# Performance work log

Hardware: AMD Instinct MI355X
Metric: run time of the kernel (lower is better)

The kernel has to match this reference:

```python
import jax, jax.numpy as jnp
import numpy as np

D_MODEL = 1024
N_HEADS = 16
D_HIDDEN = 4096
EPS = 1e-6
MASK_VAL = 1e10


def layernorm(x, gamma, beta):
    # Matches torch module: unbiased std (N-1), divide by (std + eps)
    mean = jnp.mean(x, axis=-1, keepdims=True)
    d = x.shape[-1]
    std = jnp.sqrt(jnp.sum((x - mean) ** 2, axis=-1, keepdims=True) / (d - 1))
    return gamma * (x - mean) / (std + EPS) + beta


def multihead(q_in, k_in, v_in, wq, wk, wv, wo, causal):
    # nn.Linear(bias=False): y = x @ W.T
    q = q_in @ wq.T
    k = k_in @ wk.T
    v = v_in @ wv.T
    B, Sq, D = q.shape
    Sk = k.shape[1]
    H, dh = N_HEADS, D // N_HEADS
    q = q.reshape(B, Sq, H, dh)
    k = k.reshape(B, Sk, H, dh)
    v = v.reshape(B, Sk, H, dh)
    scores = jnp.einsum('bqhd,bkhd->bhqk', q, k)  # [B,H,Sq,Sk]
    if causal:
        tri = jnp.triu(jnp.full((Sk, Sk), MASK_VAL, dtype=scores.dtype), k=1)
        scores = scores - tri  # mask applied BEFORE scaling, as in source
    scale = jnp.sqrt(jnp.asarray(D_MODEL, dtype=scores.dtype))  # d_key = d_model
    att = jax.nn.softmax(scores / scale, axis=-1)
    out = jnp.einsum('bhqk,bkhd->bqhd', att, v).reshape(B, Sq, D)
    return out @ wo.T


def setup_inputs() -> dict:
    key = jax.random.key(0)
    ks = jax.random.split(key, 24)
    B, S, D, DH = 2, 2048, D_MODEL, D_HIDDEN
    w = lambda k, shp: (jax.random.normal(k, shp, dtype=jnp.float32) * 0.02)
    inp = {
        'x': jax.random.normal(ks[0], (B, S, D), dtype=jnp.float32),
        'encoding': jax.random.normal(ks[1], (B, S, D), dtype=jnp.float32),
        'sa_wq': w(ks[2], (D, D)), 'sa_wk': w(ks[3], (D, D)),
        'sa_wv': w(ks[4], (D, D)), 'sa_wo': w(ks[5], (D, D)),
        'ca_wq': w(ks[6], (D, D)), 'ca_wk': w(ks[7], (D, D)),
        'ca_wv': w(ks[8], (D, D)), 'ca_wo': w(ks[9], (D, D)),
        'ff_w1': w(ks[10], (DH, D)), 'ff_b1': jnp.zeros((DH,), jnp.float32),
        'ff_w2': w(ks[11], (D, DH)), 'ff_b2': jnp.zeros((D,), jnp.float32),
        'ln1_g': jnp.ones((D,), jnp.float32), 'ln1_b': jnp.zeros((D,), jnp.float32),
        'ln2_g': jnp.ones((D,), jnp.float32), 'ln2_b': jnp.zeros((D,), jnp.float32),
        'ln3_g': jnp.ones((D,), jnp.float32), 'ln3_b': jnp.zeros((D,), jnp.float32),
    }
    return inp


def reference(x, encoding, sa_wq, sa_wk, sa_wv, sa_wo, ca_wq, ca_wk, ca_wv, ca_wo,
              ff_w1, ff_b1, ff_w2, ff_b2, ln1_g, ln1_b, ln2_g, ln2_b, ln3_g, ln3_b):
    # self-attention (causal) + post-norm residual
    h = layernorm(x + multihead(x, x, x, sa_wq, sa_wk, sa_wv, sa_wo, causal=True), ln1_g, ln1_b)
    # cross-attention + post-norm residual
    h = layernorm(h + multihead(h, encoding, encoding, ca_wq, ca_wk, ca_wv, ca_wo, causal=False), ln2_g, ln2_b)
    # feed-forward + post-norm residual
    ff = jax.nn.relu(h @ ff_w1.T + ff_b1) @ ff_w2.T + ff_b2
    return layernorm(h + ff, ln3_g, ln3_b)
```

## Files before the change

### kernel.cpp

```cpp
#include <hip/hip_runtime.h>
#include <hip/hip_bf16.h>
#include <math.h>

#define D_MODEL 1024
#define NHEADS  16
#define DHEAD   64
#define D_HID   4096

typedef __attribute__((ext_vector_type(8))) short short8;
typedef __attribute__((ext_vector_type(4))) short short4v;
typedef __attribute__((ext_vector_type(4))) float f32x4;
typedef __attribute__((ext_vector_type(16))) float f32x16;

#define QSCALE_F 0.04508422002778011f
#define MASK_T   4.5084220e8f

__device__ inline short f2bs(float x) {
    union { __hip_bfloat16 b; short s; } u;
    u.b = __float2bfloat16(x);
    return u.s;
}
__device__ inline float bs2f(ushort s) {
    union { unsigned u; float f; } v; v.u = ((unsigned)s) << 16; return v.f;
}
__device__ inline unsigned cvtpk(float lo, float hi) {
    unsigned r;
    asm("v_cvt_pk_bf16_f32 %0, %1, %2" : "=v"(r) : "v"(lo), "v"(hi));
    return r;
}
__device__ inline short8 pack8(float4 x, float4 y) {
    short8 v;
    v[0] = f2bs(x.x); v[1] = f2bs(x.y); v[2] = f2bs(x.z); v[3] = f2bs(x.w);
    v[4] = f2bs(y.x); v[5] = f2bs(y.y); v[6] = f2bs(y.z); v[7] = f2bs(y.w);
    return v;
}
typedef const unsigned __attribute__((address_space(1))) gu32;
typedef unsigned __attribute__((address_space(3))) lu32;
__device__ inline void gload16(const void* g, void* l) {
    __builtin_amdgcn_global_load_lds((gu32*)g, (lu32*)l, 16, 0, 0);
}
__device__ inline int swz(int r, int byteInRow) {
    return (r * 128 + byteInRow) ^ ((r & 7) << 4);
}

struct WP { const float* p[10]; };
__global__ __launch_bounds__(256) void cast_weights(WP wp, short* __restrict__ dst) {
    const int n8 = (16 << 20) / 8;
    for (int i = blockIdx.x * 256 + threadIdx.x; i < n8; i += gridDim.x * 256) {
        size_t e = (size_t)i * 8;
        int seg = (int)(e >> 20);
        const float* src;
        if (seg < 8)       src = wp.p[seg] + (e & ((1u << 20) - 1));
        else if (seg < 12) src = wp.p[8] + (e - ((size_t)8 << 20));
        else               src = wp.p[9] + (e - ((size_t)12 << 20));
        float4 a = *(const float4*)src;
        float4 b = *(const float4*)(src + 4);
        *(short8*)(dst + e) = pack8(a, b);
    }
}

__global__ __launch_bounds__(256) void cast_f2b(const float* __restrict__ in,
                                                short* __restrict__ out, int n8) {
    for (int i = blockIdx.x * 256 + threadIdx.x; i < n8; i += gridDim.x * 256) {
        float4 a = *(const float4*)(in + (size_t)i * 8);
        float4 b = *(const float4*)(in + (size_t)i * 8 + 4);
        *(short8*)(out + (size_t)i * 8) = pack8(a, b);
    }
}

template<int OM, bool BIAS, bool RELU, bool ACCUM>
__global__ __launch_bounds__(256) void gemm_mfma(
    const short* __restrict__ A, int lda,
    const short* __restrict__ Bm, int ldb,
    const float* __restrict__ bias,
    float* __restrict__ Cf, short* __restrict__ Cb, int ldc,
    int M, int N, int K, size_t routeElems, float qscale)
{
    __shared__ short Als[2][128 * 64];
    __shared__ short Bls[2][128 * 64];

    const int tid = threadIdx.x, w = tid >> 6, l = tid & 63;
    const int l15 = l & 15, lhi = l >> 4;
    const int wr = w >> 1, wc = w & 1;

    const int kh = (OM == 3) ? blockIdx.z : 0;
    if (OM == 3) {
        A  += (size_t)kh * K;
        Bm += (size_t)kh * K;
    }

    const unsigned nwg  = gridDim.x * gridDim.y;
    const unsigned wgid = blockIdx.y * gridDim.x + blockIdx.x;
    const unsigned cpx  = nwg >> 3;
    const unsigned sid  = (wgid & 7) * cpx + (wgid >> 3);
    const int bm = (int)(sid / gridDim.x) * 128;
    const int bn = (int)(sid % gridDim.x) * 128;

    const int srow = w * 8 + (l >> 3);
    const int schk = ((l & 7) ^ (l >> 3)) * 8;

    f32x4 acc[4][4] = {};

    #pragma unroll
    for (int i = 0; i < 4; ++i) {
        const short* ga = A  + (size_t)(bm + i * 32 + srow) * lda + schk;
        const short* gb = Bm + (size_t)(bn + i * 32 + srow) * ldb + schk;
        gload16(ga, &Als[0][i * 2048 + w * 512]);
        gload16(gb, &Bls[0][i * 2048 + w * 512]);
    }
    __syncthreads();

    const int nIter = K >> 6;
    int cur = 0;
    for (int it = 0; it < nIter; ++it) {
        if (it + 1 < nIter) {
            const int k1 = (it + 1) << 6;
            #pragma unroll
            for (int i = 0; i < 4; ++i) {
                const short* ga = A  + (size_t)(bm + i * 32 + srow) * lda + k1 + schk;
                const short* gb = Bm + (size_t)(bn + i * 32 + srow) * ldb + k1 + schk;
                gload16(ga, &Als[cur ^ 1][i * 2048 + w * 512]);
                gload16(gb, &Bls[cur ^ 1][i * 2048 + w * 512]);
            }
        }

        short8 af[4][2], bf[4][2];
        #pragma unroll
        for (int m = 0; m < 4; ++m) {
            const int row = wr * 64 + m * 16 + l15;
            #pragma unroll
            for (int kk = 0; kk < 2; ++kk)
                af[m][kk] = *(const short8*)&Als[cur][row * 64 + (((kk * 4 + lhi) ^ (l15 & 7)) * 8)];
        }
        #pragma unroll
        for (int n = 0; n < 4; ++n) {
            const int row = wc * 64 + n * 16 + l15;
            #pragma unroll
            for (int kk = 0; kk < 2; ++kk)
                bf[n][kk] = *(const short8*)&Bls[cur][row * 64 + (((kk * 4 + lhi) ^ (l15 & 7)) * 8)];
        }
        __builtin_amdgcn_s_setprio(1);
        #pragma unroll
        for (int kk = 0; kk < 2; ++kk)
            #pragma unroll
            for (int m = 0; m < 4; ++m)
                #pragma unroll
                for (int n = 0; n < 4; ++n)
                    acc[m][n] = __builtin_amdgcn_mfma_f32_16x16x32_bf16(af[m][kk], bf[n][kk], acc[m][n], 0, 0, 0);
        __builtin_amdgcn_s_setprio(0);

        __syncthreads();
        cur ^= 1;
    }

    #pragma unroll
    for (int n = 0; n < 4; ++n) {
        const int col = bn + wc * 64 + n * 16 + l15;
        float bv = 0.f;
        if (BIAS && (OM != 3 || kh == 0)) bv = bias[col];
        const float sc = (OM == 2) ? (col < 1024 ? qscale : 1.f) : qscale;
        #pragma unroll
        for (int m = 0; m < 4; ++m) {
            const int row0 = bm + wr * 64 + m * 16 + lhi * 4;
            #pragma unroll
            for (int i = 0; i < 4; ++i) {
                float v = acc[m][n][i] + bv;
                if (ACCUM) v += Cf[(size_t)(row0 + i) * ldc + col];
                if (RELU)  v = fmaxf(v, 0.f);
                v *= sc;
                if (OM == 0) {
                    Cf[(size_t)(row0 + i) * ldc + col] = v;
                } else if (OM == 1) {
                    Cb[(size_t)(row0 + i) * ldc + col] = f2bs(v);
                } else if (OM == 2) {
                    Cb[(size_t)(col >> 10) * routeElems +
                       (size_t)(row0 + i) * 1024 + (col & 1023)] = f2bs(v);
                } else {
                    if (kh == 0) Cf[(size_t)(row0 + i) * ldc + col] = v;
                    else         Cb[(size_t)(row0 + i) * ldc + col] = f2bs(v);
                }
            }
        }
    }
}

__global__ __launch_bounds__(256) void v_prep(
    const short* __restrict__ Vb_, short* __restrict__ Vt, int S)
{
    const int t = blockIdx.x, bh = blockIdx.y;
    const int b = bh >> 4, h = bh & 15;
    const int tid = threadIdx.x;
    const int r = tid >> 2, g = tid & 3;
    __shared__ ushort vs[64][65];

    const size_t inrow = ((size_t)b * S + t * 64 + r) * D_MODEL + h * DHEAD;
    const size_t tbase = ((size_t)bh * (S / 64) + t) * 4096;

    short8 v0 = *(const short8*)(Vb_ + inrow + g * 16);
    short8 v1 = *(const short8*)(Vb_ + inrow + g * 16 + 8);
    #pragma unroll
    for (int j = 0; j < 8; ++j) { vs[r][g * 16 + j] = (ushort)v0[j]; vs[r][g * 16 + 8 + j] = (ushort)v1[j]; }
    __syncthreads();
    short8 q0, q1;
    #pragma unroll
    for (int j = 0; j < 8; ++j) {
        q0[j] = (short)vs[g * 16 + j][r];
        q1[j] = (short)vs[g * 16 + 8 + j][r];
    }
    *(short8*)(Vt + tbase + r * 64 + g * 16)     = q0;
    *(short8*)(Vt + tbase + r * 64 + g * 16 + 8) = q1;
}

template<bool CAUSAL>
__global__ __launch_bounds__(256, 3) void attn_v11(
    const short* __restrict__ Qb, const short* __restrict__ Kr,
    const short* __restrict__ Vt, short* __restrict__ Out, int S)
{
    __shared__ __align__(16) char smem[2 * 16384];

    const int tid = threadIdx.x, w = tid >> 6, l = tid & 63;
    const int l31 = l & 31, hi = l >> 5;
    const int bnd = blockIdx.x;
    const int bh = blockIdx.y, b = bh >> 4, h = bh & 15;
    const int qw = bnd * 128 + w * 32;
    const int q  = qw + l31;

    const short* qp = Qb + ((size_t)(b * S + q)) * 1024 + h * 64 + hi * 8;
    short8 bq[4];
    #pragma unroll
    for (int dc = 0; dc < 4; ++dc) bq[dc] = *(const short8*)(qp + dc * 16);

    const short* kbase = Kr + ((size_t)b * S) * 1024 + h * 64;
    const short* vbase = Vt + (size_t)bh * ((S / 64) * 4096);

    f32x16 ot0 = {}, ot1 = {};
    float l_lane = 0.f;

    const int tMax = CAUSAL ? (2 * bnd + 1) : (S / 64 - 1);

    const int j0   = w * 2;
    const int sro  = j0 * 8 + (l >> 3);
    const int schk = ((l & 7) ^ (l >> 3)) * 8;

    {
        char* Kls = smem;  char* Vls = smem + 8192;
        gload16(kbase + (size_t)(sro)     * 1024 + schk, Kls + j0 * 1024);
        gload16(kbase + (size_t)(sro + 8) * 1024 + schk, Kls + j0 * 1024 + 1024);
        gload16(vbase + (size_t)(sro)     * 64   + schk, Vls + j0 * 1024);
        gload16(vbase + (size_t)(sro + 8) * 64   + schk, Vls + j0 * 1024 + 1024);
    }
    __syncthreads();

    int cur = 0;
    for (int t = 0; t <= tMax; ++t) {
        if (t + 1 <= tMax) {
            char* Kn = smem + (cur ^ 1) * 16384;
            char* Vn = Kn + 8192;
            const size_t krow = (size_t)((t + 1) * 64 + sro);
            const size_t vbas = (size_t)(t + 1) * 4096;
            gload16(kbase + krow * 1024 + schk,              Kn + j0 * 1024);
            gload16(kbase + (krow + 8) * 1024 + schk,        Kn + j0 * 1024 + 1024);
            gload16(vbase + vbas + (size_t)sro * 64 + schk,       Vn + j0 * 1024);
            gload16(vbase + vbas + (size_t)(sro + 8) * 64 + schk, Vn + j0 * 1024 + 1024);
        }

        const char* Kls = smem + cur * 16384;
        const char* Vls = Kls + 8192;
        const int kv0 = t * 64;

        if (!(CAUSAL && kv0 > qw + 31)) {
            f32x16 st0 = {}, st1 = {};
            __builtin_amdgcn_s_setprio(1);
            #pragma unroll
            for (int dc = 0; dc < 4; ++dc) {
                short8 a0 = *(const short8*)(Kls + swz(l31,      dc * 32 + hi * 16));
                short8 a1 = *(const short8*)(Kls + swz(32 + l31, dc * 32 + hi * 16));
                st0 = __builtin_amdgcn_mfma_f32_32x32x16_bf16(a0, bq[dc], st0, 0, 0, 0);
                st1 = __builtin_amdgcn_mfma_f32_32x32x16_bf16(a1, bq[dc], st1, 0, 0, 0);
            }
            __builtin_amdgcn_s_setprio(0);

            if (CAUSAL && kv0 + 31 > qw) {
                #pragma unroll
                for (int r = 0; r < 16; ++r) {
                    int kv = kv0 + (r & 3) + 8 * (r >> 2) + 4 * hi;
                    if (kv > q) st0[r] -= MASK_T;
                }
            }
            if (CAUSAL && kv0 + 63 > qw) {
                #pragma unroll
                for (int r = 0; r < 16; ++r) {
                    int kv = kv0 + 32 + (r & 3) + 8 * (r >> 2) + 4 * hi;
                    if (kv > q) st1[r] -= MASK_T;
                }
            }

            union U { unsigned u[4]; short8 s; };
            U c00, c01, c10, c11;
            {
                float p[16];
                #pragma unroll
                for (int r = 0; r < 16; ++r) { p[r] = __builtin_amdgcn_exp2f(st0[r]); l_lane += p[r]; }
                unsigned wd[8], sx[8];
                #pragma unroll
                for (int i = 0; i < 8; ++i) wd[i] = cvtpk(p[2 * i], p[2 * i + 1]);
                #pragma unroll
                for (int i = 0; i < 8; ++i) sx[i] = __shfl_xor(wd[i], 32, 64);
                if (hi == 0) {
                    c00.u[0] = wd[0]; c00.u[1] = wd[1]; c00.u[2] = sx[0]; c00.u[3] = sx[1];
                    c01.u[0] = wd[4]; c01.u[1] = wd[5]; c01.u[2] = sx[4]; c01.u[3] = sx[5];
                } else {
                    c00.u[0] = sx[2]; c00.u[1] = sx[3]; c00.u[2] = wd[2]; c00.u[3] = wd[3];
                    c01.u[0] = sx[6]; c01.u[1] = sx[7]; c01.u[2] = wd[6]; c01.u[3] = wd[7];
                }
            }
            {
                float p[16];
                #pragma unroll
                for (int r = 0; r < 16; ++r) { p[r] = __builtin_amdgcn_exp2f(st1[r]); l_lane += p[r]; }
                unsigned wd[8], sx[8];
                #pragma unroll
                for (int i = 0; i < 8; ++i) wd[i] = cvtpk(p[2 * i], p[2 * i + 1]);
                #pragma unroll
                for (int i = 0; i < 8; ++i) sx[i] = __shfl_xor(wd[i], 32, 64);
                if (hi == 0) {
                    c10.u[0] = wd[0]; c10.u[1] = wd[1]; c10.u[2] = sx[0]; c10.u[3] = sx[1];
                    c11.u[0] = wd[4]; c11.u[1] = wd[5]; c11.u[2] = sx[4]; c11.u[3] = sx[5];
                } else {
                    c10.u[0] = sx[2]; c10.u[1] = sx[3]; c10.u[2] = wd[2]; c10.u[3] = wd[3];
                    c11.u[0] = sx[6]; c11.u[1] = sx[7]; c11.u[2] = wd[6]; c11.u[3] = wd[7];
                }
            }

            __builtin_amdgcn_s_setprio(1);
            short8 av;
            av  = *(const short8*)(Vls + swz(l31,      hi * 16));
            ot0 = __builtin_amdgcn_mfma_f32_32x32x16_bf16(av, c00.s, ot0, 0, 0, 0);
            av  = *(const short8*)(Vls + swz(32 + l31, hi * 16));
            ot1 = __builtin_amdgcn_mfma_f32_32x32x16_bf16(av, c00.s, ot1, 0, 0, 0);
            av  = *(const short8*)(Vls + swz(l31,      32 + hi * 16));
            ot0 = __builtin_amdgcn_mfma_f32_32x32x16_bf16(av, c01.s, ot0, 0, 0, 0);
            av  = *(const short8*)(Vls + swz(32 + l31, 32 + hi * 16));
            ot1 = __builtin_amdgcn_mfma_f32_32x32x16_bf16(av, c01.s, ot1, 0, 0, 0);
            av  = *(const short8*)(Vls + swz(l31,      64 + hi * 16));
            ot0 = __builtin_amdgcn_mfma_f32_32x32x16_bf16(av, c10.s, ot0, 0, 0, 0);
            av  = *(const short8*)(Vls + swz(32 + l31, 64 + hi * 16));
            ot1 = __builtin_amdgcn_mfma_f32_32x32x16_bf16(av, c10.s, ot1, 0, 0, 0);
            av  = *(const short8*)(Vls + swz(l31,      96 + hi * 16));
            ot0 = __builtin_amdgcn_mfma_f32_32x32x16_bf16(av, c11.s, ot0, 0, 0, 0);
            av  = *(const short8*)(Vls + swz(32 + l31, 96 + hi * 16));
            ot1 = __builtin_amdgcn_mfma_f32_32x32x16_bf16(av, c11.s, ot1, 0, 0, 0);
            __builtin_amdgcn_s_setprio(0);
        }

        __syncthreads();
        cur ^= 1;
    }

    const float l_tot = l_lane + __shfl_xor(l_lane, 32, 64);
    const float inv = 1.f / l_tot;
    short* orow = Out + ((size_t)(b * S + q)) * 1024 + h * 64;
    #pragma unroll
    for (int i = 0; i < 8; ++i) {
        int dbase = ((2 * i) & 3) + 8 * (i >> 1) + 4 * hi;
        *(unsigned*)(orow + dbase)      = cvtpk(ot0[2 * i] * inv, ot0[2 * i + 1] * inv);
        *(unsigned*)(orow + 32 + dbase) = cvtpk(ot1[2 * i] * inv, ot1[2 * i + 1] * inv);
    }
}

template<bool IN1BF, bool OUTBF, bool P3>
__global__ __launch_bounds__(256) void add_ln(
    const void* __restrict__ in1, const float* __restrict__ in2,
    const short* __restrict__ in3,
    const float* __restrict__ gam, const float* __restrict__ bet,
    void* __restrict__ y)
{
    const int row = blockIdx.x;
    const int tid = threadIdx.x;
    const size_t off = (size_t)row * D_MODEL;

    float a0, a1, a2, a3;
    if (IN1BF) {
        short4v xs = ((const short4v*)((const short*)in1 + off))[tid];
        a0 = bs2f((ushort)xs[0]); a1 = bs2f((ushort)xs[1]);
        a2 = bs2f((ushort)xs[2]); a3 = bs2f((ushort)xs[3]);
    } else {
        float4 xv = ((const float4*)((const float*)in1 + off))[tid];
        a0 = xv.x; a1 = xv.y; a2 = xv.z; a3 = xv.w;
    }
    float4 rv = ((const float4*)(in2 + off))[tid];
    float v0 = a0 + rv.x, v1 = a1 + rv.y, v2 = a2 + rv.z, v3 = a3 + rv.w;
    if (P3) {
        short4v ps = ((const short4v*)(in3 + off))[tid];
        v0 += bs2f((ushort)ps[0]); v1 += bs2f((ushort)ps[1]);
        v2 += bs2f((ushort)ps[2]); v3 += bs2f((ushort)ps[3]);
    }

    float s  = v0 + v1 + v2 + v3;
    float ss = v0 * v0 + v1 * v1 + v2 * v2 + v3 * v3;

    __shared__ float sb[8];
    #pragma unroll
    for (int o = 32; o > 0; o >>= 1) {
        s  += __shfl_down(s, o, 64);
        ss += __shfl_down(ss, o, 64);
    }
    const int lane = tid & 63, w = tid >> 6;
    if (lane == 0) { sb[w] = s; sb[4 + w] = ss; }
    __syncthreads();
    float S  = sb[0] + sb[1] + sb[2] + sb[3];
    float SS = sb[4] + sb[5] + sb[6] + sb[7];

    float mean = S * (1.f / D_MODEL);
    float var_sum = SS - S * mean;
    float stdv = sqrtf(var_sum * (1.f / (D_MODEL - 1)));
    float inv = 1.f / (stdv + 1e-6f);

    float4 gv = ((const float4*)gam)[tid];
    float4 bv = ((const float4*)bet)[tid];
    float o0 = gv.x * (v0 - mean) * inv + bv.x;
    float o1 = gv.y * (v1 - mean) * inv + bv.y;
    float o2 = gv.z * (v2 - mean) * inv + bv.z;
    float o3 = gv.w * (v3 - mean) * inv + bv.w;
    if (OUTBF) {
        short4v ov; ov[0] = f2bs(o0); ov[1] = f2bs(o1); ov[2] = f2bs(o2); ov[3] = f2bs(o3);
        ((short4v*)((short*)y + off))[tid] = ov;
    } else {
        ((float4*)((float*)y + off))[tid] = make_float4(o0, o1, o2, o3);
    }
}

extern "C" void kernel_launch(void* const* d_in, const int* in_sizes, int n_in,
                              void* d_out, int out_size, void* d_ws, size_t ws_size,
                              hipStream_t stream)
{
    const float* x     = (const float*)d_in[0];
    const float* enc   = (const float*)d_in[1];
    WP wp;
    for (int i = 0; i < 8; ++i) wp.p[i] = (const float*)d_in[2 + i];
    wp.p[8] = (const float*)d_in[10];
    wp.p[9] = (const float*)d_in[12];
    const float* ff_b1 = (const float*)d_in[11];
    const float* ff_b2 = (const float*)d_in[13];
    const float* ln1_g = (const float*)d_in[14];
    const float* ln1_b = (const float*)d_in[15];
    const float* ln2_g = (const float*)d_in[16];
    const float* ln2_b = (const float*)d_in[17];
    const float* ln3_g = (const float*)d_in[18];
    const float* ln3_b = (const float*)d_in[19];
    float* out = (float*)d_out;

    const int Bn = 2, S = 2048, M = Bn * S;
    const size_t MB = 1u << 20;
    char* ws = (char*)d_ws;
    short* Wb   = (short*)(ws);
    short* p32  = (short*)(ws + 32 * MB);
    short* p40  = (short*)(ws + 40 * MB);
    short* p48  = (short*)(ws + 48 * MB);
    short* p56  = (short*)(ws + 56 * MB);
    short* p64  = (short*)(ws + 64 * MB);
    short* p72  = (short*)(ws + 72 * MB);
    float* f0   = (float*)(ws + 80 * MB);

    short* tbuf = p48;

    const size_t RT = 4 * MB;
    const short* W_saqkv = Wb;
    const short* W_sawo  = Wb + 3 * MB;
    const short* W_caq   = Wb + 4 * MB;
    const short* W_cakv  = Wb + 5 * MB;
    const short* W_cawo  = Wb + 7 * MB;
    const short* W_ff1   = Wb + 8 * MB;
    const short* W_ff2   = Wb + 12 * MB;

    dim3 blk(256);
    dim3 g_qkv(3072 / 128, M / 128);
    dim3 g_kv(2048 / 128, M / 128);
    dim3 g_n1k(1024 / 128, M / 128);
    dim3 g_spl(1024 / 128, M / 128, 2);
    dim3 g_ff1(4096 / 128, M / 128);
    dim3 g_attn(S / 128, Bn * NHEADS);
    dim3 g_vp(S / 64, Bn * NHEADS);
    dim3 g_ln(M);

    cast_weights<<<2048, blk, 0, stream>>>(wp, Wb);
    cast_f2b<<<2048, blk, 0, stream>>>(x, p32, (M * D_MODEL) / 8);

    gemm_mfma<2,false,false,false><<<g_qkv, blk, 0, stream>>>(p32, 1024, W_saqkv, 1024, nullptr, nullptr, p40, 1024, M, 3072, 1024, RT, QSCALE_F);
    v_prep<<<g_vp, blk, 0, stream>>>(p56, p72, S);
    attn_v11<true><<<g_attn, blk, 0, stream>>>(p40, p48, p72, p32, S);
    gemm_mfma<3,false,false,false><<<g_spl, blk, 0, stream>>>(p32, 1024, W_sawo, 1024, nullptr, f0, p48, 1024, M, 1024, 512, 0, 1.f);
    add_ln<false,true,true><<<g_ln, blk, 0, stream>>>(x, f0, p48, ln1_g, ln1_b, p32);

    cast_f2b<<<2048, blk, 0, stream>>>(enc, p64, (M * D_MODEL) / 8);
    gemm_mfma<2,false,false,false><<<g_kv, blk, 0, stream>>>(p64, 1024, W_cakv, 1024, nullptr, nullptr, p48, 1024, M, 2048, 1024, RT, 1.f);
    gemm_mfma<1,false,false,false><<<g_n1k, blk, 0, stream>>>(p32, 1024, W_caq, 1024, nullptr, nullptr, p40, 1024, M, 1024, 1024, 0, QSCALE_F);
    v_prep<<<g_vp, blk, 0, stream>>>(p56, p72, S);
    attn_v11<false><<<g_attn, blk, 0, stream>>>(p40, p48, p72, p56, S);
    gemm_mfma<3,false,false,false><<<g_spl, blk, 0, stream>>>(p56, 1024, W_cawo, 1024, nullptr, f0, p48, 1024, M, 1024, 512, 0, 1.f);
    add_ln<true,true,true><<<g_ln, blk, 0, stream>>>(p32, f0, p48, ln2_g, ln2_b, p40);

    gemm_mfma<1,true,true,false><<<g_ff1, blk, 0, stream>>>(p40, 1024, W_ff1, 1024, ff_b1, nullptr, tbuf, 4096, M, 4096, 1024, 0, 1.f);
    gemm_mfma<3,true,false,false><<<g_spl, blk, 0, stream>>>(tbuf, 4096, W_ff2, 4096, ff_b2, f0, p32, 1024, M, 1024, 2048, 0, 1.f);
    add_ln<true,false,true><<<g_ln, blk, 0, stream>>>(p40, f0, p32, ln3_g, ln3_b, out);
}
```

Baseline: 357.5 us.

## Switch GEMM to triple-buffered BK=32 pipeline with partial vmcnt waits

The GEMM main loop moves from a double-buffered K-tile of 64 to a triple-buffered K-tile of 32, prefetching two stages ahead. Full __syncthreads is replaced with s_waitcnt vmcnt(4) plus a raw barrier, so loads for the next stage can stay in flight across the barrier. The LDS layout packs two rows per 64-short line with a new XOR swizzle. The aim is better latency hiding, at the cost of twice as many barriers per unit of K and less MFMA work per iteration.

```diff
diff --git a/kernel.cpp b/kernel.cpp
--- a/kernel.cpp
+++ b/kernel.cpp
@@ -76,8 +76,8 @@
     float* __restrict__ Cf, short* __restrict__ Cb, int ldc,
     int M, int N, int K, size_t routeElems, float qscale)
 {
-    __shared__ short Als[2][128 * 64];
-    __shared__ short Bls[2][128 * 64];
+    __shared__ short As[3][4096];
+    __shared__ short Bs[3][4096];
 
     const int tid = threadIdx.x, w = tid >> 6, l = tid & 63;
     const int l15 = l & 15, lhi = l >> 4;
@@ -96,61 +96,76 @@
     const int bm = (int)(sid / gridDim.x) * 128;
     const int bn = (int)(sid % gridDim.x) * 128;
 
-    const int srow = w * 8 + (l >> 3);
-    const int schk = ((l & 7) ^ (l >> 3)) * 8;
+    const int sloc  = w * 8 + (l >> 3);
+    const int clog  = (l & 7) ^ ((l >> 3) & 7);
+    const int rbit  = clog >> 2;
+    const int kcol  = (clog & 3) * 8;
 
     f32x4 acc[4][4] = {};
-
-    #pragma unroll
-    for (int i = 0; i < 4; ++i) {
-        const short* ga = A  + (size_t)(bm + i * 32 + srow) * lda + schk;
-        const short* gb = Bm + (size_t)(bn + i * 32 + srow) * ldb + schk;
-        gload16(ga, &Als[0][i * 2048 + w * 512]);
-        gload16(gb, &Bls[0][i * 2048 + w * 512]);
-    }
-    __syncthreads();
-
-    const int nIter = K >> 6;
-    int cur = 0;
+    const int nIter = K >> 5;
+
+    #pragma unroll
+    for (int j = 0; j < 2; ++j) {
+        const int sr = j * 32 + sloc;
+        const int ra = 2 * sr + rbit;
+        gload16(A  + (size_t)(bm + ra) * lda + kcol, &As[0][j * 2048 + w * 512]);
+        gload16(Bm + (size_t)(bn + ra) * ldb + kcol, &Bs[0][j * 2048 + w * 512]);
+    }
+    #pragma unroll
+    for (int j = 0; j < 2; ++j) {
+        const int sr = j * 32 + sloc;
+        const int ra = 2 * sr + rbit;
+        gload16(A  + (size_t)(bm + ra) * lda + 32 + kcol, &As[1][j * 2048 + w * 512]);
+        gload16(Bm + (size_t)(bn + ra) * ldb + 32 + kcol, &Bs[1][j * 2048 + w * 512]);
+    }
+    asm volatile("s_waitcnt vmcnt(4)" ::: "memory");
+    __builtin_amdgcn_s_barrier();
+
+    int cur = 0, nxt2 = 2;
     for (int it = 0; it < nIter; ++it) {
-        if (it + 1 < nIter) {
-            const int k1 = (it + 1) << 6;
+        if (it + 2 < nIter) {
+            const int k0 = (it + 2) << 5;
             #pragma unroll
-            for (int i = 0; i < 4; ++i) {
-                const short* ga = A  + (size_t)(bm + i * 32 + srow) * lda + k1 + schk;
-                const short* gb = Bm + (size_t)(bn + i * 32 + srow) * ldb + k1 + schk;
-                gload16(ga, &Als[cur ^ 1][i * 2048 + w * 512]);
-                gload16(gb, &Bls[cur ^ 1][i * 2048 + w * 512]);
-            }
-        }
-
-        short8 af[4][2], bf[4][2];
+            for (int j = 0; j < 2; ++j) {
+                const int sr = j * 32 + sloc;
+                const int ra = 2 * sr + rbit;
+                gload16(A  + (size_t)(bm + ra) * lda + k0 + kcol, &As[nxt2][j * 2048 + w * 512]);
+                gload16(Bm + (size_t)(bn + ra) * ldb + k0 + kcol, &Bs[nxt2][j * 2048 + w * 512]);
+            }
+        }
+
+        short8 af[4], bf[4];
         #pragma unroll
         for (int m = 0; m < 4; ++m) {
-            const int row = wr * 64 + m * 16 + l15;
-            #pragma unroll
-            for (int kk = 0; kk < 2; ++kk)
-                af[m][kk] = *(const short8*)&Als[cur][row * 64 + (((kk * 4 + lhi) ^ (l15 & 7)) * 8)];
+            const int r = wr * 64 + m * 16 + l15;
+            const int s = r >> 1;
+            const int c = (((r & 1) << 2) | lhi) ^ (s & 7);
+            af[m] = *(const short8*)&As[cur][s * 64 + c * 8];
         }
         #pragma unroll
         for (int n = 0; n < 4; ++n) {
-            const int row = wc * 64 + n * 16 + l15;
-            #pragma unroll
-            for (int kk = 0; kk < 2; ++kk)
-                bf[n][kk] = *(const short8*)&Bls[cur][row * 64 + (((kk * 4 + lhi) ^ (l15 & 7)) * 8)];
+            const int r = wc * 64 + n * 16 + l15;
+            const int s = r >> 1;
+            const int c = (((r & 1) << 2) | lhi) ^ (s & 7);
+            bf[n] = *(const short8*)&Bs[cur][s * 64 + c * 8];
         }
         __builtin_amdgcn_s_setprio(1);
         #pragma unroll
-        for (int kk = 0; kk < 2; ++kk)
+        for (int m = 0; m < 4; ++m)
             #pragma unroll
-            for (int m = 0; m < 4; ++m)
-                #pragma unroll
-                for (int n = 0; n < 4; ++n)
-                    acc[m][n] = __builtin_amdgcn_mfma_f32_16x16x32_bf16(af[m][kk], bf[n][kk], acc[m][n], 0, 0, 0);
+            for (int n = 0; n < 4; ++n)
+                acc[m][n] = __builtin_amdgcn_mfma_f32_16x16x32_bf16(af[m], bf[n], acc[m][n], 0, 0, 0);
         __builtin_amdgcn_s_setprio(0);
 
-        __syncthreads();
-        cur ^= 1;
+        if (it + 2 < nIter) {
+            asm volatile("s_waitcnt vmcnt(4)" ::: "memory");
+            __builtin_amdgcn_s_barrier();
+        } else if (it + 1 < nIter) {
+            asm volatile("s_waitcnt vmcnt(0)" ::: "memory");
+            __builtin_amdgcn_s_barrier();
+        }
+        cur = (cur == 2) ? 0 : cur + 1;
+        nxt2 = (nxt2 == 2) ? 0 : nxt2 + 1;
     }
 
     #pragma unroll
```

Result: slower. 388.4 us (+8.6%).
